# Kernel tuning notes

Hardware: AMD Instinct MI355X
Metric: run time of the kernel (lower is better)

Reference implementation:

```python
import jax, jax.numpy as jnp
import numpy as np

B, D_IN, D_H, D_OUT = 16384, 1024, 4096, 1024
EPS = 1e-5  # nn.LayerNorm default


def setup_inputs() -> dict:
    key = jax.random.key(0)
    k1, k2, k3, k4, k5, k6 = jax.random.split(key, 6)
    s1 = 1.0 / np.sqrt(D_IN)
    s2 = 1.0 / np.sqrt(D_H)
    return {
        "embedding": jax.random.normal(k1, (B, D_IN), dtype=jnp.float32),
        "W1": jax.random.uniform(k2, (D_IN, D_H), minval=-s1, maxval=s1, dtype=jnp.float32),
        "b1": jax.random.uniform(k3, (D_H,), minval=-s1, maxval=s1, dtype=jnp.float32),
        "ln_gamma": jnp.ones((D_H,), dtype=jnp.float32),
        "ln_beta": jnp.zeros((D_H,), dtype=jnp.float32),
        "W2": jax.random.uniform(k4, (D_H, D_OUT), minval=-s2, maxval=s2, dtype=jnp.float32),
    }


def reference(embedding, W1, b1, ln_gamma, ln_beta, W2) -> jnp.ndarray:
    # Linear 1
    h = embedding @ W1 + b1  # [B, D_H]
    # LayerNorm over last dim
    mu = jnp.mean(h, axis=-1, keepdims=True)
    var = jnp.mean(jnp.square(h - mu), axis=-1, keepdims=True)
    h = (h - mu) * jax.lax.rsqrt(var + EPS) * ln_gamma + ln_beta
    # Exact GELU (torch nn.GELU default uses erf)
    h = jax.nn.gelu(h, approximate=False)
    # Linear 2 (no bias)
    return h @ W2  # [B, D_OUT]
```

## Files before the change

kernel.cpp:

```cpp
#include <hip/hip_runtime.h>
#include <hip/hip_bf16.h>
#include <math.h>


typedef unsigned short ushort_t;
typedef __bf16 bf16x8 __attribute__((ext_vector_type(8)));
typedef float f32x4 __attribute__((ext_vector_type(4)));

__device__ __forceinline__ ushort_t f2bf(float f) {
  unsigned u = __builtin_bit_cast(unsigned, f);
  u += 0x7FFFu + ((u >> 16) & 1u);
  return (ushort_t)(u >> 16);
}

__device__ __forceinline__ void gload_lds16(const void* g, void* l) {
  __builtin_amdgcn_global_load_lds(
      (const __attribute__((address_space(1))) void*)g,
      (__attribute__((address_space(3))) void*)l, 16, 0, 0);
}

__global__ void __launch_bounds__(256) cast_kernel(const float* __restrict__ in,
                                                   ushort_t* __restrict__ out,
                                                   long n) {
  long i = ((long)blockIdx.x * 256 + threadIdx.x) * 4;
  const long stride = (long)gridDim.x * 256 * 4;
  for (; i < n; i += stride) {
    float4 v = *(const float4*)(in + i);
    ushort4 o;
    o.x = f2bf(v.x); o.y = f2bf(v.y); o.z = f2bf(v.z); o.w = f2bf(v.w);
    *(ushort4*)(out + i) = o;
  }
}

__global__ void __launch_bounds__(256) transpose_cast(const float* __restrict__ in,
                                                      ushort_t* __restrict__ out,
                                                      int R, int C) {
  __shared__ float tile[32][33];
  const int bx = blockIdx.x * 32;
  const int by = blockIdx.y * 32;
  const int tx = threadIdx.x;
  const int ty = threadIdx.y;
#pragma unroll
  for (int i = 0; i < 32; i += 8)
    tile[ty + i][tx] = in[(long)(by + ty + i) * C + (bx + tx)];
  __syncthreads();
#pragma unroll
  for (int i = 0; i < 32; i += 8)
    out[(long)(bx + ty + i) * R + (by + tx)] = f2bf(tile[tx][ty + i]);
}

template <int EPI>
__global__ void __launch_bounds__(256) gemm_bt(const ushort_t* __restrict__ A,
                                               const ushort_t* __restrict__ Bt,
                                               const float* __restrict__ bias,
                                               void* __restrict__ Cout,
                                               int N, int K, int nbn) {
  __shared__ ushort_t As[128 * 32];
  __shared__ ushort_t Bs[128 * 32];
  const int tid = threadIdx.x;
  const int lane = tid & 63;
  const int wid = tid >> 6;
  const int wr = wid >> 1;
  const int wc = wid & 1;

  const int nwg = gridDim.x;
  const int cpx = nwg >> 3;
  const int tile = (blockIdx.x & 7) * cpx + (blockIdx.x >> 3);
  const long bm = (long)(tile / nbn) * 128;
  const long bn = (long)(tile % nbn) * 128;

  f32x4 acc[4][4] = {};

  const ushort_t* Ag = A + (bm + (tid >> 2)) * (long)K + (tid & 3) * 8;
  const ushort_t* Bg = Bt + (bn + (tid >> 2)) * (long)K + (tid & 3) * 8;
  ushort_t* AsW = &As[tid * 8];
  ushort_t* BsW = &Bs[tid * 8];

  const int aOff = (wr * 64 + (lane & 15)) * 32 + (lane >> 4) * 8;
  const int bOff = (wc * 64 + (lane & 15)) * 32 + (lane >> 4) * 8;

  for (int k0 = 0; k0 < K; k0 += 32) {
    gload_lds16(Ag + k0, AsW);
    gload_lds16(Ag + (long)64 * K + k0, AsW + 2048);
    gload_lds16(Bg + k0, BsW);
    gload_lds16(Bg + (long)64 * K + k0, BsW + 2048);
    __syncthreads();

    bf16x8 af[4], bfv[4];
#pragma unroll
    for (int i = 0; i < 4; ++i) af[i] = *(const bf16x8*)&As[aOff + i * 16 * 32];
#pragma unroll
    for (int j = 0; j < 4; ++j) bfv[j] = *(const bf16x8*)&Bs[bOff + j * 16 * 32];
#pragma unroll
    for (int i = 0; i < 4; ++i)
#pragma unroll
      for (int j = 0; j < 4; ++j)
        acc[i][j] = __builtin_amdgcn_mfma_f32_16x16x32_bf16(af[i], bfv[j],
                                                            acc[i][j], 0, 0, 0);
    __syncthreads();
  }

  const long r0 = bm + wr * 64 + (lane >> 4) * 4;
  const long c0 = bn + wc * 64 + (lane & 15);
  if (EPI == 0) {
    ushort_t* C = (ushort_t*)Cout;
#pragma unroll
    for (int j = 0; j < 4; ++j) {
      const long col = c0 + j * 16;
      const float bv = bias[col];
#pragma unroll
      for (int i = 0; i < 4; ++i)
#pragma unroll
        for (int r = 0; r < 4; ++r)
          C[(r0 + i * 16 + r) * N + col] = f2bf(acc[i][j][r] + bv);
    }
  } else {
    float* C = (float*)Cout;
#pragma unroll
    for (int j = 0; j < 4; ++j) {
      const long col = c0 + j * 16;
#pragma unroll
      for (int i = 0; i < 4; ++i)
#pragma unroll
        for (int r = 0; r < 4; ++r)
          C[(r0 + i * 16 + r) * N + col] = acc[i][j][r];
    }
  }
}

__global__ void __launch_bounds__(256) ln_gelu(ushort_t* __restrict__ h,
                                               const float* __restrict__ gamma,
                                               const float* __restrict__ beta) {
  const int D = 4096;
  ushort_t* p = h + (long)blockIdx.x * D + threadIdx.x * 16;
  uint4 u0 = *(const uint4*)p;
  uint4 u1 = *(const uint4*)(p + 8);
  unsigned w[8] = {u0.x, u0.y, u0.z, u0.w, u1.x, u1.y, u1.z, u1.w};
  float x[16];
#pragma unroll
  for (int k = 0; k < 8; ++k) {
    x[2 * k]     = __builtin_bit_cast(float, w[k] << 16);
    x[2 * k + 1] = __builtin_bit_cast(float, w[k] & 0xFFFF0000u);
  }
  float s = 0.f, q = 0.f;
#pragma unroll
  for (int k = 0; k < 16; ++k) { s += x[k]; q += x[k] * x[k]; }
#pragma unroll
  for (int m = 1; m < 64; m <<= 1) {
    s += __shfl_xor(s, m, 64);
    q += __shfl_xor(q, m, 64);
  }
  __shared__ float rs[4], rq[4];
  const int wid = threadIdx.x >> 6;
  if ((threadIdx.x & 63) == 0) { rs[wid] = s; rq[wid] = q; }
  __syncthreads();
  s = rs[0] + rs[1] + rs[2] + rs[3];
  q = rq[0] + rq[1] + rq[2] + rq[3];
  const float mu = s * (1.f / 4096.f);
  const float var = q * (1.f / 4096.f) - mu * mu;
  const float rstd = rsqrtf(var + 1e-5f);

  const int cb = threadIdx.x * 16;
  float gm[16], bt[16];
#pragma unroll
  for (int k = 0; k < 4; ++k) {
    *(float4*)&gm[k * 4] = *(const float4*)&gamma[cb + k * 4];
    *(float4*)&bt[k * 4] = *(const float4*)&beta[cb + k * 4];
  }
  unsigned o[8];
#pragma unroll
  for (int k = 0; k < 16; ++k) {
    float y = (x[k] - mu) * rstd * gm[k] + bt[k];
    float z = -1.5957691216f * __builtin_fmaf(0.044715f * y, y * y, y);
    float g = y * __builtin_amdgcn_rcpf(1.f + __expf(z));
    ushort_t b = f2bf(g);
    if (k & 1) o[k >> 1] |= ((unsigned)b) << 16; else o[k >> 1] = (unsigned)b;
  }
  uint4 v0, v1;
  v0.x = o[0]; v0.y = o[1]; v0.z = o[2]; v0.w = o[3];
  v1.x = o[4]; v1.y = o[5]; v1.z = o[6]; v1.w = o[7];
  *(uint4*)p = v0;
  *(uint4*)(p + 8) = v1;
}

extern "C" void kernel_launch(void* const* d_in, const int* in_sizes, int n_in,
                              void* d_out, int out_size, void* d_ws, size_t ws_size,
                              hipStream_t stream) {
  const float* emb   = (const float*)d_in[0];
  const float* W1    = (const float*)d_in[1];
  const float* b1    = (const float*)d_in[2];
  const float* gamma = (const float*)d_in[3];
  const float* beta  = (const float*)d_in[4];
  const float* W2    = (const float*)d_in[5];
  float* out = (float*)d_out;

  const int B = 16384, DIN = 1024, DH = 4096, DOUT = 1024;
  char* ws = (char*)d_ws;
  ushort_t* h    = (ushort_t*)(ws);
  ushort_t* embB = (ushort_t*)(ws + 134217728);
  ushort_t* w1t  = (ushort_t*)(ws + 167772160);
  ushort_t* w2t  = (ushort_t*)(ws + 176160768);

  cast_kernel<<<4096, 256, 0, stream>>>(emb, embB, (long)B * DIN);
  transpose_cast<<<dim3(DH / 32, DIN / 32), dim3(32, 8), 0, stream>>>(W1, w1t, DIN, DH);
  transpose_cast<<<dim3(DOUT / 32, DH / 32), dim3(32, 8), 0, stream>>>(W2, w2t, DH, DOUT);
  gemm_bt<0><<<(B / 128) * (DH / 128), 256, 0, stream>>>(embB, w1t, b1, h, DH, DIN, DH / 128);
  ln_gelu<<<B, 256, 0, stream>>>(h, gamma, beta);
  gemm_bt<1><<<(B / 128) * (DOUT / 128), 256, 0, stream>>>(h, w2t, nullptr, out, DOUT, DH, DOUT / 128);
}
```

Measured before the change: 583.6 us.

## Replace 128x128 GEMM with pipelined 256x256 tile, swizzled LDS, double buffering

Both GEMMs move to a 256x256 output tile computed by 512 threads, with a BK=64 double-buffered LDS pipeline. Each quarter-phase issues global-to-LDS prefetches of the next tile while MFMAs run on the current one, using XOR-swizzled LDS addressing to avoid bank conflicts and s_setprio to favour the MFMA stream. The aim is to raise arithmetic intensity per tile and hide memory latency behind compute, replacing the old single-buffered loop that synchronised twice per 32-wide K step. The cost is 128KB of LDS per block plus heavy register pressure, which could reduce occupancy, and the hand-written waitcnt and barrier ordering must stay correct.

```diff
diff --git a/kernel.cpp b/kernel.cpp
--- a/kernel.cpp
+++ b/kernel.cpp
@@ -49,58 +49,123 @@
     out[(long)(bx + ty + i) * R + (by + tx)] = f2bf(tile[tx][ty + i]);
 }
 
+
+__device__ __forceinline__ void stage_half(ushort_t* dst, const ushort_t* gRow,
+                                           long K, int tid, int rS, int kbS) {
+  gload_lds16(gRow + (long)rS * K + kbS * 8, dst + (size_t)tid * 8);
+  gload_lds16(gRow + (long)(rS + 64) * K + kbS * 8, dst + (size_t)(512 + tid) * 8);
+}
+
+template <int Q, bool LOADB, bool VMW>
+__device__ __forceinline__ void phase(f32x4 (&acc)[8][4], bf16x8 (&b)[4][2],
+                                      const ushort_t* aT, const ushort_t* bT,
+                                      int rowA, int rowB, int kHi,
+                                      const ushort_t* pfSrc, ushort_t* pfDst,
+                                      long K, int tid, int rS, int kbS) {
+  if (LOADB) {
+#pragma unroll
+    for (int j = 0; j < 4; ++j) {
+      const int row = rowB + j * 16;
+      const int sw = row & 7;
+#pragma unroll
+      for (int s = 0; s < 2; ++s)
+        b[j][s] = *(const bf16x8*)(bT + row * 64 + ((s * 4 + kHi) ^ sw) * 8);
+    }
+  }
+  bf16x8 a[2][2];
+#pragma unroll
+  for (int di = 0; di < 2; ++di) {
+    const int row = rowA + (2 * Q + di) * 16;
+    const int sw = row & 7;
+#pragma unroll
+    for (int s = 0; s < 2; ++s)
+      a[di][s] = *(const bf16x8*)(aT + row * 64 + ((s * 4 + kHi) ^ sw) * 8);
+  }
+  stage_half(pfDst, pfSrc, K, tid, rS, kbS);
+  asm volatile("" ::: "memory");
+  __builtin_amdgcn_s_barrier();
+  asm volatile("s_waitcnt lgkmcnt(0)" ::: "memory");
+  __builtin_amdgcn_s_setprio(1);
+#pragma unroll
+  for (int di = 0; di < 2; ++di)
+#pragma unroll
+    for (int s = 0; s < 2; ++s)
+#pragma unroll
+      for (int j = 0; j < 4; ++j)
+        acc[2 * Q + di][j] = __builtin_amdgcn_mfma_f32_16x16x32_bf16(
+            a[di][s], b[j][s], acc[2 * Q + di][j], 0, 0, 0);
+  __builtin_amdgcn_s_setprio(0);
+  if (VMW) asm volatile("s_waitcnt vmcnt(4)" ::: "memory");
+  asm volatile("" ::: "memory");
+  __builtin_amdgcn_s_barrier();
+  asm volatile("" ::: "memory");
+}
+
 template <int EPI>
-__global__ void __launch_bounds__(256) gemm_bt(const ushort_t* __restrict__ A,
-                                               const ushort_t* __restrict__ Bt,
-                                               const float* __restrict__ bias,
-                                               void* __restrict__ Cout,
-                                               int N, int K, int nbn) {
-  __shared__ ushort_t As[128 * 32];
-  __shared__ ushort_t Bs[128 * 32];
+__global__ void __launch_bounds__(512, 2) gemm256(const ushort_t* __restrict__ A,
+                                                  const ushort_t* __restrict__ Bt,
+                                                  const float* __restrict__ bias,
+                                                  void* __restrict__ Cout,
+                                                  int N, int K, int nbn) {
+  __shared__ __align__(16) ushort_t lds[65536];
   const int tid = threadIdx.x;
   const int lane = tid & 63;
   const int wid = tid >> 6;
-  const int wr = wid >> 1;
-  const int wc = wid & 1;
+  const int wr = wid >> 2;
+  const int wc = wid & 3;
 
   const int nwg = gridDim.x;
   const int cpx = nwg >> 3;
   const int tile = (blockIdx.x & 7) * cpx + (blockIdx.x >> 3);
-  const long bm = (long)(tile / nbn) * 128;
-  const long bn = (long)(tile % nbn) * 128;
-
-  f32x4 acc[4][4] = {};
-
-  const ushort_t* Ag = A + (bm + (tid >> 2)) * (long)K + (tid & 3) * 8;
-  const ushort_t* Bg = Bt + (bn + (tid >> 2)) * (long)K + (tid & 3) * 8;
-  ushort_t* AsW = &As[tid * 8];
-  ushort_t* BsW = &Bs[tid * 8];
-
-  const int aOff = (wr * 64 + (lane & 15)) * 32 + (lane >> 4) * 8;
-  const int bOff = (wc * 64 + (lane & 15)) * 32 + (lane >> 4) * 8;
-
-  for (int k0 = 0; k0 < K; k0 += 32) {
-    gload_lds16(Ag + k0, AsW);
-    gload_lds16(Ag + (long)64 * K + k0, AsW + 2048);
-    gload_lds16(Bg + k0, BsW);
-    gload_lds16(Bg + (long)64 * K + k0, BsW + 2048);
-    __syncthreads();
-
-    bf16x8 af[4], bfv[4];
-#pragma unroll
-    for (int i = 0; i < 4; ++i) af[i] = *(const bf16x8*)&As[aOff + i * 16 * 32];
-#pragma unroll
-    for (int j = 0; j < 4; ++j) bfv[j] = *(const bf16x8*)&Bs[bOff + j * 16 * 32];
-#pragma unroll
-    for (int i = 0; i < 4; ++i)
-#pragma unroll
-      for (int j = 0; j < 4; ++j)
-        acc[i][j] = __builtin_amdgcn_mfma_f32_16x16x32_bf16(af[i], bfv[j],
-                                                            acc[i][j], 0, 0, 0);
-    __syncthreads();
-  }
-
-  const long r0 = bm + wr * 64 + (lane >> 4) * 4;
+  const long bm = (long)(tile / nbn) * 256;
+  const long bn = (long)(tile % nbn) * 256;
+
+  ushort_t* A0 = lds;
+  ushort_t* A1 = lds + 16384;
+  ushort_t* B0 = lds + 32768;
+  ushort_t* B1 = lds + 49152;
+
+  const ushort_t* Arow = A + bm * (long)K;
+  const ushort_t* Brow = Bt + bn * (long)K;
+
+  const int rS = tid >> 3;
+  const int kbS = (tid & 7) ^ (rS & 7);
+  const int rowA = wr * 128 + (lane & 15);
+  const int rowB = wc * 64 + (lane & 15);
+  const int kHi = lane >> 4;
+
+  f32x4 acc[8][4] = {};
+  bf16x8 bfr[4][2];
+
+  stage_half(A0, Arow, K, tid, rS, kbS);
+  stage_half(A0 + 8192, Arow + 128L * K, K, tid, rS, kbS);
+  stage_half(B0, Brow, K, tid, rS, kbS);
+  stage_half(B0 + 8192, Brow + 128L * K, K, tid, rS, kbS);
+  stage_half(B1, Brow + 64, K, tid, rS, kbS);
+  stage_half(B1 + 8192, Brow + 128L * K + 64, K, tid, rS, kbS);
+  asm volatile("s_waitcnt vmcnt(0)" ::: "memory");
+  __builtin_amdgcn_s_barrier();
+  asm volatile("" ::: "memory");
+
+  const int NI = K >> 7;
+  const int tmask = 2 * NI - 1;
+#pragma unroll 1
+  for (int i = 0; i < NI; ++i) {
+    const int t1 = 2 * i + 1;
+    const int t2 = (2 * i + 2) & tmask;
+    const int t3 = (2 * i + 3) & tmask;
+    phase<0, true , false>(acc, bfr, A0, B0, rowA, rowB, kHi, Arow + (long)t1 * 64,            A1,        K, tid, rS, kbS);
+    phase<1, false, false>(acc, bfr, A0, B0, rowA, rowB, kHi, Arow + 128L * K + (long)t1 * 64, A1 + 8192, K, tid, rS, kbS);
+    phase<2, false, false>(acc, bfr, A0, B0, rowA, rowB, kHi, Brow + (long)t2 * 64,            B0,        K, tid, rS, kbS);
+    phase<3, false, true >(acc, bfr, A0, B0, rowA, rowB, kHi, Brow + 128L * K + (long)t2 * 64, B0 + 8192, K, tid, rS, kbS);
+    phase<0, true , false>(acc, bfr, A1, B1, rowA, rowB, kHi, Arow + (long)t2 * 64,            A0,        K, tid, rS, kbS);
+    phase<1, false, false>(acc, bfr, A1, B1, rowA, rowB, kHi, Arow + 128L * K + (long)t2 * 64, A0 + 8192, K, tid, rS, kbS);
+    phase<2, false, false>(acc, bfr, A1, B1, rowA, rowB, kHi, Brow + (long)t3 * 64,            B1,        K, tid, rS, kbS);
+    phase<3, false, true >(acc, bfr, A1, B1, rowA, rowB, kHi, Brow + 128L * K + (long)t3 * 64, B1 + 8192, K, tid, rS, kbS);
+  }
+  asm volatile("s_waitcnt vmcnt(0)" ::: "memory");
+
+  const long r0 = bm + wr * 128 + (lane >> 4) * 4;
   const long c0 = bn + wc * 64 + (lane & 15);
   if (EPI == 0) {
     ushort_t* C = (ushort_t*)Cout;
@@ -109,10 +174,10 @@
       const long col = c0 + j * 16;
       const float bv = bias[col];
 #pragma unroll
-      for (int i = 0; i < 4; ++i)
+      for (int i2 = 0; i2 < 8; ++i2)
 #pragma unroll
         for (int r = 0; r < 4; ++r)
-          C[(r0 + i * 16 + r) * N + col] = f2bf(acc[i][j][r] + bv);
+          C[(r0 + i2 * 16 + r) * N + col] = f2bf(acc[i2][j][r] + bv);
     }
   } else {
     float* C = (float*)Cout;
@@ -120,10 +185,10 @@
     for (int j = 0; j < 4; ++j) {
       const long col = c0 + j * 16;
 #pragma unroll
-      for (int i = 0; i < 4; ++i)
+      for (int i2 = 0; i2 < 8; ++i2)
 #pragma unroll
         for (int r = 0; r < 4; ++r)
-          C[(r0 + i * 16 + r) * N + col] = acc[i][j][r];
+          C[(r0 + i2 * 16 + r) * N + col] = acc[i2][j][r];
     }
   }
 }
@@ -204,7 +269,7 @@
   cast_kernel<<<4096, 256, 0, stream>>>(emb, embB, (long)B * DIN);
   transpose_cast<<<dim3(DH / 32, DIN / 32), dim3(32, 8), 0, stream>>>(W1, w1t, DIN, DH);
   transpose_cast<<<dim3(DOUT / 32, DH / 32), dim3(32, 8), 0, stream>>>(W2, w2t, DH, DOUT);
-  gemm_bt<0><<<(B / 128) * (DH / 128), 256, 0, stream>>>(embB, w1t, b1, h, DH, DIN, DH / 128);
+  gemm256<0><<<(B / 256) * (DH / 256), 512, 0, stream>>>(embB, w1t, b1, h, DH, DIN, DH / 256);
   ln_gelu<<<B, 256, 0, stream>>>(h, gamma, beta);
-  gemm_bt<1><<<(B / 128) * (DOUT / 128), 256, 0, stream>>>(h, w2t, nullptr, out, DOUT, DH, DOUT / 128);
-}
+  gemm256<1><<<(B / 256) * (DOUT / 256), 512, 0, stream>>>(h, w2t, nullptr, out, DOUT, DH, DOUT / 256);
+}
```

New measurement: 469.8 us. 19.5% less time.
